# Kernel tuning notes

Hardware: AMD Instinct MI355X
Metric: run time of the kernel (lower is better)

## Reference

```python
import jax, jax.numpy as jnp
import numpy as np

K = 1024
D = 256
BETA = 0.25
DECAY = 0.99
EPS = 1e-05


def setup_inputs() -> dict:
    key = jax.random.key(0)
    k1, k2, k3, k4 = jax.random.split(key, 4)
    z_e = jax.random.normal(k1, (32, 2048, D), dtype=jnp.float32)
    emb = jax.random.normal(k2, (K, D), dtype=jnp.float32)
    # module L2-normalizes the codebook rows at init
    emb = emb / jnp.linalg.norm(emb, axis=1, keepdims=True)
    cluster_size = jax.random.uniform(k3, (K,), dtype=jnp.float32)
    embed_avg = jax.random.normal(k4, (K, D), dtype=jnp.float32)
    return {"z_e": z_e, "embedding": emb, "cluster_size": cluster_size, "embed_avg": embed_avg}


def reference(z_e, embedding, cluster_size, embed_avg):
    B, T, d = z_e.shape
    z = z_e.reshape(-1, d)                                   # [N, D]
    # squared-distance matrix: ||z||^2 - 2 z E^T + ||e||^2   -> [N, K]
    z_sq = jnp.sum(z * z, axis=1, keepdims=True)
    e_sq = jnp.sum(embedding * embedding, axis=1)[None, :]
    dist = z_sq - 2.0 * (z @ embedding.T) + e_sq
    codes = jnp.argmin(dist, axis=1)                         # [N]
    z_q = embedding[codes].reshape(z_e.shape)                # gather + reshape

    # ---- EMA codebook update (training branch, no-grad in torch) ----
    # scatter-reduce instead of materializing the [N, K] one-hot
    cs_batch = jax.ops.segment_sum(jnp.ones_like(codes, dtype=z.dtype), codes, num_segments=K)
    embed_sum = jax.ops.segment_sum(z, codes, num_segments=K)          # [K, D]
    new_cluster_size = cluster_size * DECAY + cs_batch * (1.0 - DECAY)
    new_embed_avg = embed_avg * DECAY + embed_sum * (1.0 - DECAY)
    n = jnp.sum(new_cluster_size)
    cs_smoothed = (new_cluster_size + EPS) / (n + K * EPS) * n
    new_embedding = new_embed_avg / cs_smoothed[:, None]

    commit_loss = jnp.mean((z_e - z_q) ** 2)
    vq_loss = BETA * commit_loss
    z_q_st = z_e + (z_q - z_e)  # straight-through (identical values in fwd)
    return (z_q_st, vq_loss, codes.reshape(B, T), new_embedding, new_cluster_size, new_embed_avg)
```

## Files before the change

### kernel.cpp

```cpp
#include <hip/hip_runtime.h>


#define DDIM 256
#define DQ   64
#define KC   1024
#define NROW 65536
#define BM   128
#define BN   128
#define BD   32
#define LS   34
#define DECAYF 0.99f
#define OMDF   0.01f
#define BETAF  0.25f
#define EPSF   1e-5f

#define BMR  128
#define NIT  24

typedef _Float16 f16;
typedef _Float16 f16x8 __attribute__((ext_vector_type(8)));
typedef float    f32x4 __attribute__((ext_vector_type(4)));

__device__ __forceinline__ void gl_lds16(const f16* g, f16* l) {
    __builtin_amdgcn_global_load_lds(
        (const __attribute__((address_space(1))) void*)g,
        (__attribute__((address_space(3))) void*)l, 16, 0, 0);
}

__global__ __launch_bounds__(256) void vq_esq(const float* __restrict__ emb,
                                              float* __restrict__ esq_g)
{
    int k = blockIdx.x * 256 + threadIdx.x;
    const float4* ep = (const float4*)(emb + (size_t)k * DDIM);
    float s = 0.f;
    for (int q = 0; q < DQ; ++q) {
        float4 v = ep[q];
        s += v.x * v.x + v.y * v.y + v.z * v.z + v.w * v.w;
    }
    esq_g[k] = s;
}

__global__ __launch_bounds__(256) void vq_prep(const float* __restrict__ src,
                                               f16* __restrict__ dst,
                                               float* __restrict__ sq_g)
{
    int t   = blockIdx.x * 256 + threadIdx.x;
    int row = t >> 5;
    int c   = t & 31;
    const float4* sp = (const float4*)(src + (size_t)row * DDIM + c * 8);
    float4 v0 = sp[0], v1 = sp[1];
    float x[8] = {v0.x, v0.y, v0.z, v0.w, v1.x, v1.y, v1.z, v1.w};
    f16x8 h, l;
    float s = 0.f;
#pragma unroll
    for (int j = 0; j < 8; ++j) {
        float xs = x[j] * 128.0f;
        f16 hh = (f16)xs;
        h[j] = hh;
        l[j] = (f16)(xs - (float)hh);
        s += x[j] * x[j];
    }
    f16* rp = dst + (size_t)row * 512;
    *(f16x8*)(rp + c * 8)       = h;
    *(f16x8*)(rp + 256 + c * 8) = l;
    s += __shfl_xor(s, 1);
    s += __shfl_xor(s, 2);
    s += __shfl_xor(s, 4);
    s += __shfl_xor(s, 8);
    s += __shfl_xor(s, 16);
    if (c == 0) sq_g[row] = s;
}

__global__ __launch_bounds__(256) void vq_prep_e(const float* __restrict__ emb,
                                                 f16* __restrict__ ehl2,
                                                 float* __restrict__ esq_g)
{
    int t     = blockIdx.x * 256 + threadIdx.x;
    int c     = t >> 5;
    int chunk = t & 31;
    const float4* sp = (const float4*)(emb + (size_t)c * DDIM + chunk * 8);
    float4 v0 = sp[0], v1 = sp[1];
    float x[8] = {v0.x, v0.y, v0.z, v0.w, v1.x, v1.y, v1.z, v1.w};
    f16x8 h, l;
    float s = 0.f;
#pragma unroll
    for (int j = 0; j < 8; ++j) {
        float xs = x[j] * 128.0f;
        f16 hh = (f16)xs;
        h[j] = hh;
        l[j] = (f16)(xs - (float)hh);
        s += x[j] * x[j];
    }
    int kb = chunk >> 2, kg = chunk & 3;
    int cg = c >> 4;
    int lanep = kg * 16 + (c & 15);
    size_t idx = ((size_t)(kb * 64 + cg)) * 512 + lanep * 8;
    *(f16x8*)(ehl2 + idx)          = h;
    *(f16x8*)(ehl2 + 262144 + idx) = l;
    s += __shfl_xor(s, 1);
    s += __shfl_xor(s, 2);
    s += __shfl_xor(s, 4);
    s += __shfl_xor(s, 8);
    s += __shfl_xor(s, 16);
    if (chunk == 0) esq_g[c] = s;
}


#define ASTAGE(b_, s_) do {                                                 \
    int off_ = (((s_) >= 8) ? 256 : 0) + ((s_) & 3) * 64;                   \
    gl_lds16(asrc0 + off_, &Abuf[b_][0] + tid * 8);                         \
    gl_lds16(asrc1 + off_, &Abuf[b_][0] + (tid + 512) * 8);                 \
} while (0)

#define BLOAD(dst_, it_, ks_) do {                                          \
    int itc_ = (it_) > NIT - 1 ? NIT - 1 : (it_);                           \
    int ps_ = itc_ / 12, sb_ = itc_ % 12;                                   \
    int pl_ = (sb_ >= 4 && sb_ < 8) ? 1 : 0;                                \
    int kb_ = (sb_ & 3) * 2 + (ks_);                                        \
    const f16* bp_ = ehl2 + (((pl_ * 8 + kb_) * 64 + ps_ * 32 + wc * 8) << 9) \
                   + lane * 8;                                              \
    _Pragma("unroll")                                                       \
    for (int j_ = 0; j_ < 8; ++j_) dst_[j_] = *(const f16x8*)(bp_ + j_ * 512); \
} while (0)

#define MM(bank_, Ab_, ks_) do {                                            \
    f16x8 a0_ = *(const f16x8*)((Ab_) + aoff[0][ks_]);                      \
    f16x8 a1_ = *(const f16x8*)((Ab_) + aoff[1][ks_]);                      \
    f16x8 a2_ = *(const f16x8*)((Ab_) + aoff[2][ks_]);                      \
    f16x8 a3_ = *(const f16x8*)((Ab_) + aoff[3][ks_]);                      \
    __builtin_amdgcn_s_setprio(1);                                          \
    _Pragma("unroll")                                                       \
    for (int j_ = 0; j_ < 8; ++j_) {                                        \
        acc[0][j_] = __builtin_amdgcn_mfma_f32_16x16x32_f16(a0_, bank_[j_], acc[0][j_], 0, 0, 0); \
        acc[1][j_] = __builtin_amdgcn_mfma_f32_16x16x32_f16(a1_, bank_[j_], acc[1][j_], 0, 0, 0); \
        acc[2][j_] = __builtin_amdgcn_mfma_f32_16x16x32_f16(a2_, bank_[j_], acc[2][j_], 0, 0, 0); \
        acc[3][j_] = __builtin_amdgcn_mfma_f32_16x16x32_f16(a3_, bank_[j_], acc[3][j_], 0, 0, 0); \
    }                                                                       \
    __builtin_amdgcn_s_setprio(0);                                          \
} while (0)

#define FOLD(P) do {                                                        \
    _Pragma("unroll")                                                       \
    for (int i_ = 0; i_ < 4; ++i_) {                                        \
      _Pragma("unroll")                                                     \
      for (int t_ = 0; t_ < 4; ++t_) {                                      \
        int row_ = wr * 64 + i_ * 16 + kg * 4 + t_;                         \
        float zq2_ = zsq_s[row_];                                           \
        float bv_ = 3.4e38f; int bix_ = 0;                                  \
        _Pragma("unroll")                                                   \
        for (int j_ = 0; j_ < 8; ++j_) {                                    \
          int col_ = (P) * 512 + wc * 128 + j_ * 16 + c16;                  \
          float d_ = fmaf(acc[i_][j_][t_], -0x1p-13f, zq2_) + esq_s[col_];  \
          if (d_ < bv_) { bv_ = d_; bix_ = col_; }                          \
        }                                                                   \
        _Pragma("unroll")                                                   \
        for (int m_ = 1; m_ < 16; m_ <<= 1) {                               \
          float ov_ = __shfl_xor(bv_, m_);                                  \
          int   oi_ = __shfl_xor(bix_, m_);                                 \
          if (ov_ < bv_ || (ov_ == bv_ && oi_ < bix_)) { bv_ = ov_; bix_ = oi_; } \
        }                                                                   \
        if (c16 == 0) {                                                     \
          red_v[row_ * 9 + (P) * 4 + wc] = bv_;                             \
          red_i[row_ * 9 + (P) * 4 + wc] = bix_;                            \
        }                                                                   \
      }                                                                     \
    }                                                                       \
    _Pragma("unroll")                                                       \
    for (int i_ = 0; i_ < 4; ++i_)                                          \
      _Pragma("unroll")                                                     \
      for (int j_ = 0; j_ < 8; ++j_) acc[i_][j_] = zero4;                   \
} while (0)

__global__ __launch_bounds__(512) void vq_main_mfma(
    const f16*  __restrict__ zhl,
    const f16*  __restrict__ ehl2,
    const float* __restrict__ esq_g,
    const float* __restrict__ zsq_g,
    float* __restrict__ out_codes)
{
    __shared__ f16   Abuf[3][8192];
    __shared__ float esq_s[KC];
    __shared__ float zsq_s[BMR];
    __shared__ float red_v[BMR * 9];
    __shared__ int   red_i[BMR * 9];

    const int tid  = threadIdx.x;
    const int row0 = blockIdx.x * BMR;
    const int wave = tid >> 6, lane = tid & 63;
    const int wr   = wave >> 2, wc = wave & 3;
    const int kg   = lane >> 4, c16 = lane & 15;

    { float2 v = ((const float2*)esq_g)[tid];
      *(float2*)(esq_s + tid * 2) = v; }
    if (tid < BMR) zsq_s[tid] = zsq_g[row0 + tid];

    const int ar = tid >> 3, ach = tid & 7;
    const f16* asrc0 = zhl + (size_t)(row0 + ar) * 512 + (ach ^ (ar & 7)) * 8;
    const f16* asrc1 = asrc0 + (size_t)64 * 512;

    int aoff[4][2];
#pragma unroll
    for (int i = 0; i < 4; ++i)
#pragma unroll
        for (int ks = 0; ks < 2; ++ks)
            aoff[i][ks] = (wr * 64 + i * 16 + c16) * 64
                        + (((ks * 4 + kg) ^ (c16 & 7)) * 8);

    f16x8 b0[8], b1[8];
    ASTAGE(0, 0);
    ASTAGE(1, 1);
    BLOAD(b0, 0, 0);
    asm volatile("s_waitcnt lgkmcnt(0)" ::: "memory");
    asm volatile("s_waitcnt vmcnt(10)" ::: "memory");
    __builtin_amdgcn_s_barrier();

    f32x4 acc[4][8];
    const f32x4 zero4 = {0.f, 0.f, 0.f, 0.f};
#pragma unroll
    for (int i = 0; i < 4; ++i)
#pragma unroll
        for (int j = 0; j < 8; ++j) acc[i][j] = zero4;

#pragma unroll 1
    for (int it = 0; it < NIT; ++it) {
        const f16* Ab = &Abuf[it % 3][0];
        BLOAD(b1, it, 1);
        MM(b0, Ab, 0);
        BLOAD(b0, it + 1, 0);
        {
            int its = it + 2;
            int bd  = its % 3;
            int ssv = (its > NIT - 1 ? NIT - 1 : its) % 12;
            ASTAGE(bd, ssv);
        }
        MM(b1, Ab, 1);
        if ((it % 12) == 11) { FOLD(it / 12); }
        asm volatile("s_waitcnt vmcnt(18)" ::: "memory");
        __builtin_amdgcn_s_barrier();
    }

    __syncthreads();
    if (tid < BMR) {
        float bv = red_v[tid * 9];
        int   bi = red_i[tid * 9];
#pragma unroll
        for (int t = 1; t < 8; ++t) {
            float v  = red_v[tid * 9 + t];
            int   ix = red_i[tid * 9 + t];
            if (v < bv || (v == bv && ix < bi)) { bv = v; bi = ix; }
        }
        out_codes[row0 + tid] = (float)bi;
    }
}

__global__ __launch_bounds__(256) void vq_epi(
    const float* __restrict__ z,
    const float* __restrict__ emb,
    const float* __restrict__ codes_f,
    float* __restrict__ out_zq,
    float* __restrict__ loss_acc)
{
    __shared__ int   codes_s[64];
    __shared__ float lred[256];
    const int tid  = threadIdx.x;
    const int row0 = blockIdx.x * 64;
    const int wave = tid >> 6, lane = tid & 63;

    if (tid < 64) codes_s[tid] = (int)codes_f[row0 + tid];
    __syncthreads();

    float lp = 0.f;
#pragma unroll 1
    for (int r = wave; r < 64; r += 4) {
        int code = codes_s[r];
        float4 e4 = *(const float4*)(emb + (size_t)code * DDIM + lane * 4);
        float4 z4 = *(const float4*)(z + (size_t)(row0 + r) * DDIM + lane * 4);
        float dx = e4.x - z4.x, dy = e4.y - z4.y, dz = e4.z - z4.z, dw = e4.w - z4.w;
        float4 o;
        o.x = z4.x + dx; o.y = z4.y + dy; o.z = z4.z + dz; o.w = z4.w + dw;
        *(float4*)(out_zq + (size_t)(row0 + r) * DDIM + lane * 4) = o;
        lp += dx * dx + dy * dy + dz * dz + dw * dw;
    }
    lred[tid] = lp;
    __syncthreads();
    for (int s = 128; s > 0; s >>= 1) {
        if (tid < s) lred[tid] += lred[tid + s];
        __syncthreads();
    }
    if (tid == 0) atomicAdd(loss_acc, lred[0]);
}

__global__ __launch_bounds__(256) void vq_main_f32(
    const float* __restrict__ z,
    const float* __restrict__ emb,
    const float* __restrict__ esq_g,
    float* __restrict__ out_zq,
    float* __restrict__ out_codes,
    float* __restrict__ loss_acc)
{
    __shared__ float zs[BM * LS];
    __shared__ float es[BN * LS];
    __shared__ float esq_s[KC];
    __shared__ float zsq_s[BM];
    float* red_v   = zs;
    int*   red_i   = (int*)(zs + 2048);
    int*   codes_s = (int*)es;
    float* lred    = es + 128;

    const int tid  = threadIdx.x;
    const int row0 = blockIdx.x * BM;
    const int trow = tid >> 4;
    const int tcol = tid & 15;

    {
        const float4* eg = (const float4*)esq_g;
        float4 v = eg[tid];
        *(float4*)(esq_s + tid * 4) = v;
    }
    if (tid < BM) {
        const float4* zp = (const float4*)(z + (size_t)(row0 + tid) * DDIM);
        float s = 0.f;
        for (int q = 0; q < DQ; ++q) {
            float4 v = zp[q];
            s += v.x * v.x + v.y * v.y + v.z * v.z + v.w * v.w;
        }
        zsq_s[tid] = s;
    }

    const int r0 = tid >> 3;
    const int q0 = tid & 7;
    const float* zp0 = z + (size_t)(row0 + r0) * DDIM + q0 * 4;
    const float* ep0 = emb + (size_t)r0 * DDIM + q0 * 4;
    const int ls0 = r0 * LS + q0 * 4;

    float4 pz[4], pe[4];
#pragma unroll
    for (int it = 0; it < 4; ++it) {
        pz[it] = *(const float4*)(zp0 + it * 32 * DDIM);
        pe[it] = *(const float4*)(ep0 + it * 32 * DDIM);
    }

    float runv[8];
    int   runi[8];
#pragma unroll
    for (int i = 0; i < 8; ++i) { runv[i] = 3.4e38f; runi[i] = 0; }

#pragma unroll 1
    for (int kt = 0; kt < KC / BN; ++kt) {
        float acc[8][8];
#pragma unroll
        for (int i = 0; i < 8; ++i)
#pragma unroll
            for (int j = 0; j < 8; ++j) acc[i][j] = 0.f;

#pragma unroll 1
        for (int dc = 0; dc < DDIM / BD; ++dc) {
            __syncthreads();
#pragma unroll
            for (int it = 0; it < 4; ++it) {
                int o = ls0 + it * 32 * LS;
                *(float2*)(zs + o)     = make_float2(pz[it].x, pz[it].y);
                *(float2*)(zs + o + 2) = make_float2(pz[it].z, pz[it].w);
                *(float2*)(es + o)     = make_float2(pe[it].x, pe[it].y);
                *(float2*)(es + o + 2) = make_float2(pe[it].z, pe[it].w);
            }
            __syncthreads();
            {
                int ndc = dc + 1, nkt = kt;
                if (ndc == DDIM / BD) { ndc = 0; ++nkt; }
                if (nkt < KC / BN) {
                    size_t zo = (size_t)ndc * BD;
                    size_t eo = (size_t)nkt * BN * DDIM + (size_t)ndc * BD;
#pragma unroll
                    for (int it = 0; it < 4; ++it) {
                        pz[it] = *(const float4*)(zp0 + it * 32 * DDIM + zo);
                        pe[it] = *(const float4*)(ep0 + it * 32 * DDIM + eo);
                    }
                }
            }
#pragma unroll
            for (int s = 0; s < BD / 2; ++s) {
                float2 a2[8], b2[8];
#pragma unroll
                for (int i = 0; i < 8; ++i)
                    a2[i] = *(const float2*)(zs + (trow + 16 * i) * LS + s * 2);
#pragma unroll
                for (int j = 0; j < 8; ++j)
                    b2[j] = *(const float2*)(es + (tcol + 16 * j) * LS + s * 2);
#pragma unroll
                for (int i = 0; i < 8; ++i)
#pragma unroll
                    for (int j = 0; j < 8; ++j)
                        acc[i][j] = fmaf(a2[i].y, b2[j].y,
                                     fmaf(a2[i].x, b2[j].x, acc[i][j]));
            }
        }
#pragma unroll
        for (int i = 0; i < 8; ++i) {
            float zq2 = zsq_s[trow + 16 * i];
#pragma unroll
            for (int j = 0; j < 8; ++j) {
                int col = kt * BN + tcol + 16 * j;
                float dist = zq2 - 2.f * acc[i][j] + esq_s[col];
                if (dist < runv[i]) { runv[i] = dist; runi[i] = col; }
            }
        }
    }

    __syncthreads();
#pragma unroll
    for (int i = 0; i < 8; ++i) {
        int lr = trow + 16 * i;
        red_v[lr * 16 + tcol] = runv[i];
        red_i[lr * 16 + tcol] = runi[i];
    }
    __syncthreads();
    if (tid < BM) {
        float bv = red_v[tid * 16];
        int   bi = red_i[tid * 16];
        for (int t = 1; t < 16; ++t) {
            float v  = red_v[tid * 16 + t];
            int   ix = red_i[tid * 16 + t];
            if (v < bv || (v == bv && ix < bi)) { bv = v; bi = ix; }
        }
        codes_s[tid] = bi;
        out_codes[row0 + tid] = (float)bi;
    }
    __syncthreads();

    const int wavf = tid >> 6;
    const int lanf = tid & 63;
    float lp = 0.f;
    for (int r = wavf; r < BM; r += 4) {
        int code = codes_s[r];
        float4 e4 = *(const float4*)(emb + (size_t)code * DDIM + lanf * 4);
        float4 z4 = *(const float4*)(z + (size_t)(row0 + r) * DDIM + lanf * 4);
        float dx = e4.x - z4.x, dy = e4.y - z4.y, dz = e4.z - z4.z, dw = e4.w - z4.w;
        float4 o;
        o.x = z4.x + dx; o.y = z4.y + dy; o.z = z4.z + dz; o.w = z4.w + dw;
        *(float4*)(out_zq + (size_t)(row0 + r) * DDIM + lanf * 4) = o;
        lp += dx * dx + dy * dy + dz * dz + dw * dw;
    }
    lred[tid] = lp;
    __syncthreads();
    for (int s = 128; s > 0; s >>= 1) {
        if (tid < s) lred[tid] += lred[tid + s];
        __syncthreads();
    }
    if (tid == 0) atomicAdd(loss_acc, lred[0]);
}

__global__ __launch_bounds__(256) void vq_scatter(
    const float* __restrict__ z,
    const float* __restrict__ codes_f,
    float* __restrict__ embed_sum,
    float* __restrict__ counts)
{
    __shared__ int list[1024];
    __shared__ int nmatch;
    const int k   = blockIdx.x;
    const int tid = threadIdx.x;

    float acc = 0.f;
    int total = 0;
    if (tid == 0) nmatch = 0;
    __syncthreads();

    for (int base = 0; base < NROW; base += 1024) {
        float4 c4 = *(const float4*)(codes_f + base + tid * 4);
        int i0 = base + tid * 4;
        if ((int)c4.x == k) { int p = atomicAdd(&nmatch, 1); list[p] = i0; }
        if ((int)c4.y == k) { int p = atomicAdd(&nmatch, 1); list[p] = i0 + 1; }
        if ((int)c4.z == k) { int p = atomicAdd(&nmatch, 1); list[p] = i0 + 2; }
        if ((int)c4.w == k) { int p = atomicAdd(&nmatch, 1); list[p] = i0 + 3; }
        __syncthreads();
        int nm = nmatch;
        for (int i = 0; i < nm; ++i)
            acc += z[(size_t)list[i] * DDIM + tid];
        total += nm;
        __syncthreads();
        if (tid == 0) nmatch = 0;
        __syncthreads();
    }
    embed_sum[(size_t)k * DDIM + tid] = acc;
    if (tid == 0) counts[k] = (float)total;
}

__global__ void vq_finalize(const float* __restrict__ cluster_size,
                            const float* __restrict__ counts,
                            const float* __restrict__ loss_acc,
                            float* __restrict__ out_ncs,
                            float* __restrict__ out_loss,
                            float* __restrict__ cs_sm,
                            float inv_ND)
{
    __shared__ float sred[KC];
    const int tid = threadIdx.x;
    float ncs = cluster_size[tid] * DECAYF + counts[tid] * OMDF;
    out_ncs[tid] = ncs;
    sred[tid] = ncs;
    __syncthreads();
    for (int s = KC / 2; s > 0; s >>= 1) {
        if (tid < s) sred[tid] += sred[tid + s];
        __syncthreads();
    }
    float n = sred[0];
    cs_sm[tid] = (ncs + EPSF) / (n + (float)KC * EPSF) * n;
    if (tid == 0) out_loss[0] = BETAF * loss_acc[0] * inv_ND;
}

__global__ void vq_embed(const float* __restrict__ embed_avg,
                         const float* __restrict__ embed_sum,
                         const float* __restrict__ cs_sm,
                         float* __restrict__ out_nea,
                         float* __restrict__ out_nemb)
{
    int idx = blockIdx.x * blockDim.x + threadIdx.x;
    int k = idx >> 6;
    float4 ea = ((const float4*)embed_avg)[idx];
    float4 s4 = ((const float4*)embed_sum)[idx];
    float4 nea;
    nea.x = ea.x * DECAYF + s4.x * OMDF;
    nea.y = ea.y * DECAYF + s4.y * OMDF;
    nea.z = ea.z * DECAYF + s4.z * OMDF;
    nea.w = ea.w * DECAYF + s4.w * OMDF;
    ((float4*)out_nea)[idx] = nea;
    float cs = cs_sm[k];
    float4 ne;
    ne.x = nea.x / cs; ne.y = nea.y / cs; ne.z = nea.z / cs; ne.w = nea.w / cs;
    ((float4*)out_nemb)[idx] = ne;
}

extern "C" void kernel_launch(void* const* d_in, const int* in_sizes, int n_in,
                              void* d_out, int out_size, void* d_ws, size_t ws_size,
                              hipStream_t stream) {
    const float* z            = (const float*)d_in[0];
    const float* emb          = (const float*)d_in[1];
    const float* cluster_size = (const float*)d_in[2];
    const float* embed_avg    = (const float*)d_in[3];

    const int ND = in_sizes[0];
    const int KD = in_sizes[1];
    const int K  = in_sizes[2];
    const int N  = ND / DDIM;

    float* out       = (float*)d_out;
    float* out_zq    = out;
    float* out_loss  = out + (size_t)ND;
    float* out_codes = out + (size_t)ND + 1;
    float* out_nemb  = out + (size_t)ND + 1 + N;
    float* out_ncs   = out_nemb + (size_t)KD;
    float* out_nea   = out_ncs + (size_t)K;

    float* ws        = (float*)d_ws;
    float* loss_acc  = ws;
    float* counts    = ws + 1;
    float* cs_sm     = counts + K;
    float* esq_g     = cs_sm + K;
    float* zsq_g     = esq_g + K;
    float* embed_sum = zsq_g + N;

    size_t base_floats = (size_t)1 + 3 * (size_t)K + (size_t)N + (size_t)KD;
    size_t f16_off = (base_floats * sizeof(float) + 255) & ~(size_t)255;
    size_t zbytes  = (size_t)N * 512 * sizeof(f16);
    size_t ebytes  = (size_t)2 * 262144 * sizeof(f16);
    bool mfma_ok   = ws_size >= f16_off + zbytes + ebytes;

    hipMemsetAsync(loss_acc, 0, sizeof(float), stream);
    if (mfma_ok) {
        f16* zhl  = (f16*)((char*)d_ws + f16_off);
        f16* ehl2 = (f16*)((char*)d_ws + f16_off + zbytes);
        vq_prep<<<(N * 32) / 256, 256, 0, stream>>>(z, zhl, zsq_g);
        vq_prep_e<<<(K * 32) / 256, 256, 0, stream>>>(emb, ehl2, esq_g);
        vq_main_mfma<<<N / BMR, 512, 0, stream>>>(
            zhl, ehl2, esq_g, zsq_g, out_codes);
        vq_epi<<<N / 64, 256, 0, stream>>>(z, emb, out_codes, out_zq, loss_acc);
    } else {
        vq_esq<<<K / 256, 256, 0, stream>>>(emb, esq_g);
        vq_main_f32<<<N / BM, 256, 0, stream>>>(z, emb, esq_g,
                                                out_zq, out_codes, loss_acc);
    }
    vq_scatter<<<K, 256, 0, stream>>>(z, out_codes, embed_sum, counts);
    vq_finalize<<<1, K, 0, stream>>>(cluster_size, counts, loss_acc,
                                     out_ncs, out_loss, cs_sm, 1.0f / (float)ND);
    vq_embed<<<KD / 1024, 256, 0, stream>>>(embed_avg, embed_sum, cs_sm,
                                            out_nea, out_nemb);
}
```

Before: 353.4 us.

## Give each wave all 128 rows and a narrower code slice, double-buffer A

The wave-to-tile mapping changes from a 2x4 grid (64 rows x 128 codes per wave) to 1x8 (all 128 rows x 64 codes per wave). Each wave now reads half as much codebook data from global memory per step but twice as many A fragments from LDS. The A staging buffer goes from triple to double buffering, with the next stage issued at the top of each iteration and the vmcnt waits adjusted to match. The partial argmin reduction now collects 16 candidates per row in a transposed layout, which trades less LDS use and global B traffic for more LDS reads and a shallower prefetch.

```diff
diff --git a/kernel.cpp b/kernel.cpp
--- a/kernel.cpp
+++ b/kernel.cpp
@@ -117,10 +117,11 @@
     int ps_ = itc_ / 12, sb_ = itc_ % 12;                                   \
     int pl_ = (sb_ >= 4 && sb_ < 8) ? 1 : 0;                                \
     int kb_ = (sb_ & 3) * 2 + (ks_);                                        \
-    const f16* bp_ = ehl2 + (((pl_ * 8 + kb_) * 64 + ps_ * 32 + wc * 8) << 9) \
-                   + lane * 8;                                              \
+    const f16* bp_ = ehl2 + (((size_t)((pl_ * 8 + kb_) * 64 + ps_ * 32      \
+                   + wc * 4)) << 9) + lane * 8;                             \
     _Pragma("unroll")                                                       \
-    for (int j_ = 0; j_ < 8; ++j_) dst_[j_] = *(const f16x8*)(bp_ + j_ * 512); \
+    for (int j_ = 0; j_ < 4; ++j_)                                          \
+        dst_[j_] = *(const f16x8*)(bp_ + ((size_t)j_ << 9));                \
 } while (0)
 
 #define MM(bank_, Ab_, ks_) do {                                            \
@@ -128,28 +129,36 @@
     f16x8 a1_ = *(const f16x8*)((Ab_) + aoff[1][ks_]);                      \
     f16x8 a2_ = *(const f16x8*)((Ab_) + aoff[2][ks_]);                      \
     f16x8 a3_ = *(const f16x8*)((Ab_) + aoff[3][ks_]);                      \
+    f16x8 a4_ = *(const f16x8*)((Ab_) + aoff[4][ks_]);                      \
+    f16x8 a5_ = *(const f16x8*)((Ab_) + aoff[5][ks_]);                      \
+    f16x8 a6_ = *(const f16x8*)((Ab_) + aoff[6][ks_]);                      \
+    f16x8 a7_ = *(const f16x8*)((Ab_) + aoff[7][ks_]);                      \
     __builtin_amdgcn_s_setprio(1);                                          \
     _Pragma("unroll")                                                       \
-    for (int j_ = 0; j_ < 8; ++j_) {                                        \
+    for (int j_ = 0; j_ < 4; ++j_) {                                        \
         acc[0][j_] = __builtin_amdgcn_mfma_f32_16x16x32_f16(a0_, bank_[j_], acc[0][j_], 0, 0, 0); \
         acc[1][j_] = __builtin_amdgcn_mfma_f32_16x16x32_f16(a1_, bank_[j_], acc[1][j_], 0, 0, 0); \
         acc[2][j_] = __builtin_amdgcn_mfma_f32_16x16x32_f16(a2_, bank_[j_], acc[2][j_], 0, 0, 0); \
         acc[3][j_] = __builtin_amdgcn_mfma_f32_16x16x32_f16(a3_, bank_[j_], acc[3][j_], 0, 0, 0); \
+        acc[4][j_] = __builtin_amdgcn_mfma_f32_16x16x32_f16(a4_, bank_[j_], acc[4][j_], 0, 0, 0); \
+        acc[5][j_] = __builtin_amdgcn_mfma_f32_16x16x32_f16(a5_, bank_[j_], acc[5][j_], 0, 0, 0); \
+        acc[6][j_] = __builtin_amdgcn_mfma_f32_16x16x32_f16(a6_, bank_[j_], acc[6][j_], 0, 0, 0); \
+        acc[7][j_] = __builtin_amdgcn_mfma_f32_16x16x32_f16(a7_, bank_[j_], acc[7][j_], 0, 0, 0); \
     }                                                                       \
     __builtin_amdgcn_s_setprio(0);                                          \
 } while (0)
 
 #define FOLD(P) do {                                                        \
     _Pragma("unroll")                                                       \
-    for (int i_ = 0; i_ < 4; ++i_) {                                        \
+    for (int i_ = 0; i_ < 8; ++i_) {                                        \
       _Pragma("unroll")                                                     \
       for (int t_ = 0; t_ < 4; ++t_) {                                      \
-        int row_ = wr * 64 + i_ * 16 + kg * 4 + t_;                         \
+        int row_ = i_ * 16 + kg * 4 + t_;                                   \
         float zq2_ = zsq_s[row_];                                           \
         float bv_ = 3.4e38f; int bix_ = 0;                                  \
         _Pragma("unroll")                                                   \
-        for (int j_ = 0; j_ < 8; ++j_) {                                    \
-          int col_ = (P) * 512 + wc * 128 + j_ * 16 + c16;                  \
+        for (int j_ = 0; j_ < 4; ++j_) {                                    \
+          int col_ = (P) * 512 + wc * 64 + j_ * 16 + c16;                   \
           float d_ = fmaf(acc[i_][j_][t_], -0x1p-13f, zq2_) + esq_s[col_];  \
           if (d_ < bv_) { bv_ = d_; bix_ = col_; }                          \
         }                                                                   \
@@ -160,15 +169,15 @@
           if (ov_ < bv_ || (ov_ == bv_ && oi_ < bix_)) { bv_ = ov_; bix_ = oi_; } \
         }                                                                   \
         if (c16 == 0) {                                                     \
-          red_v[row_ * 9 + (P) * 4 + wc] = bv_;                             \
-          red_i[row_ * 9 + (P) * 4 + wc] = bix_;                            \
+          red_v[((P) * 8 + wc) * 128 + row_] = bv_;                         \
+          red_i[((P) * 8 + wc) * 128 + row_] = bix_;                        \
         }                                                                   \
       }                                                                     \
     }                                                                       \
     _Pragma("unroll")                                                       \
-    for (int i_ = 0; i_ < 4; ++i_)                                          \
+    for (int i_ = 0; i_ < 8; ++i_)                                          \
       _Pragma("unroll")                                                     \
-      for (int j_ = 0; j_ < 8; ++j_) acc[i_][j_] = zero4;                   \
+      for (int j_ = 0; j_ < 4; ++j_) acc[i_][j_] = zero4;                   \
 } while (0)
 
 __global__ __launch_bounds__(512) void vq_main_mfma(
@@ -178,16 +187,16 @@
     const float* __restrict__ zsq_g,
     float* __restrict__ out_codes)
 {
-    __shared__ f16   Abuf[3][8192];
+    __shared__ f16   Abuf[2][8192];
     __shared__ float esq_s[KC];
     __shared__ float zsq_s[BMR];
-    __shared__ float red_v[BMR * 9];
-    __shared__ int   red_i[BMR * 9];
+    __shared__ float red_v[16 * BMR];
+    __shared__ int   red_i[16 * BMR];
 
     const int tid  = threadIdx.x;
     const int row0 = blockIdx.x * BMR;
     const int wave = tid >> 6, lane = tid & 63;
-    const int wr   = wave >> 2, wc = wave & 3;
+    const int wc   = wave;
     const int kg   = lane >> 4, c16 = lane & 15;
 
     { float2 v = ((const float2*)esq_g)[tid];
@@ -198,55 +207,52 @@
     const f16* asrc0 = zhl + (size_t)(row0 + ar) * 512 + (ach ^ (ar & 7)) * 8;
     const f16* asrc1 = asrc0 + (size_t)64 * 512;
 
-    int aoff[4][2];
-#pragma unroll
-    for (int i = 0; i < 4; ++i)
+    int aoff[8][2];
+#pragma unroll
+    for (int i = 0; i < 8; ++i)
 #pragma unroll
         for (int ks = 0; ks < 2; ++ks)
-            aoff[i][ks] = (wr * 64 + i * 16 + c16) * 64
+            aoff[i][ks] = (i * 16 + c16) * 64
                         + (((ks * 4 + kg) ^ (c16 & 7)) * 8);
 
-    f16x8 b0[8], b1[8];
+    f16x8 b0[4], b1[4];
     ASTAGE(0, 0);
-    ASTAGE(1, 1);
     BLOAD(b0, 0, 0);
-    asm volatile("s_waitcnt lgkmcnt(0)" ::: "memory");
-    asm volatile("s_waitcnt vmcnt(10)" ::: "memory");
+    asm volatile("s_waitcnt vmcnt(0) lgkmcnt(0)" ::: "memory");
     __builtin_amdgcn_s_barrier();
 
-    f32x4 acc[4][8];
+    f32x4 acc[8][4];
     const f32x4 zero4 = {0.f, 0.f, 0.f, 0.f};
 #pragma unroll
-    for (int i = 0; i < 4; ++i)
-#pragma unroll
-        for (int j = 0; j < 8; ++j) acc[i][j] = zero4;
+    for (int i = 0; i < 8; ++i)
+#pragma unroll
+        for (int j = 0; j < 4; ++j) acc[i][j] = zero4;
 
 #pragma unroll 1
     for (int it = 0; it < NIT; ++it) {
-        const f16* Ab = &Abuf[it % 3][0];
+        const f16* Ab = &Abuf[it & 1][0];
+        if (it < NIT - 1) {
+            int its = it + 1;
+            ASTAGE(its & 1, its % 12);
+        }
+        __builtin_amdgcn_sched_barrier(0);
         BLOAD(b1, it, 1);
         MM(b0, Ab, 0);
         BLOAD(b0, it + 1, 0);
-        {
-            int its = it + 2;
-            int bd  = its % 3;
-            int ssv = (its > NIT - 1 ? NIT - 1 : its) % 12;
-            ASTAGE(bd, ssv);
-        }
         MM(b1, Ab, 1);
         if ((it % 12) == 11) { FOLD(it / 12); }
-        asm volatile("s_waitcnt vmcnt(18)" ::: "memory");
+        asm volatile("s_waitcnt vmcnt(8)" ::: "memory");
         __builtin_amdgcn_s_barrier();
     }
 
     __syncthreads();
     if (tid < BMR) {
-        float bv = red_v[tid * 9];
-        int   bi = red_i[tid * 9];
-#pragma unroll
-        for (int t = 1; t < 8; ++t) {
-            float v  = red_v[tid * 9 + t];
-            int   ix = red_i[tid * 9 + t];
+        float bv = red_v[tid];
+        int   bi = red_i[tid];
+#pragma unroll
+        for (int t = 1; t < 16; ++t) {
+            float v  = red_v[t * 128 + tid];
+            int   ix = red_i[t * 128 + tid];
             if (v < bv || (v == bv && ix < bi)) { bv = v; bi = ix; }
         }
         out_codes[row0 + tid] = (float)bi;
```

Result: slower. 365.2 us (+3.4%).
